# Performance work log

Hardware: AMD Instinct MI355X
Metric: run time of the kernel (lower is better)

Reference implementation:

```python
import jax, jax.numpy as jnp
import numpy as np

# --- module hyperparameters (init_kwargs) ---
K = 64
PZ, PY, PX = 5, 5, 5          # patch_size
PROJ = 512                     # projection_dim
B, C, D, H, W = 4, 256, 32, 64, 64


def setup_inputs() -> dict:
    key = jax.random.key(0)
    k1, k2, k3, k4 = jax.random.split(key, 4)
    feature_map = jax.random.normal(k1, (B, C, D, H, W), jnp.float32)
    score_map = jax.random.normal(k2, (B, 1, D, H, W), jnp.float32)
    # LazyLinear(projection_dim) materialized: in_features = C * K
    Wp = jax.random.normal(k3, (PROJ, C * K), jnp.float32) / np.sqrt(C * K).astype(np.float32)
    b = jax.random.normal(k4, (PROJ,), jnp.float32) * 0.01
    return {"feature_map": feature_map, "score_map": score_map, "Wp": Wp, "b": b}


def reference(feature_map, score_map, Wp, b):
    Bn, Cn, Dn, Hn, Wn = feature_map.shape
    flat = score_map.reshape(Bn, -1)                      # (B, D*H*W)
    scores, idx = jax.lax.top_k(flat, K)                  # (B, K)
    z = idx // (Hn * Wn)
    y = (idx % (Hn * Wn)) // Wn
    x = idx % Wn
    centers = jnp.stack([z, y, x], axis=-1)               # (B, K, 3)

    # boundary-clamped window origins: z0 = max(cz - dz//2, 0), window [z0, min(z0+dz, D))
    z0 = jnp.maximum(z - PZ // 2, 0)
    y0 = jnp.maximum(y - PY // 2, 0)
    x0 = jnp.maximum(x - PX // 2, 0)

    def per_batch(fm, z0b, y0b, x0b):
        # fm: (C, D, H, W); z0b/y0b/x0b: (K,)
        iz = z0b[:, None] + jnp.arange(PZ)                # (K, PZ)
        iy = y0b[:, None] + jnp.arange(PY)
        ix = x0b[:, None] + jnp.arange(PX)
        mz, my, mx = iz < Dn, iy < Hn, ix < Wn            # out-of-range => excluded from mean
        iz = jnp.minimum(iz, Dn - 1)
        iy = jnp.minimum(iy, Hn - 1)
        ix = jnp.minimum(ix, Wn - 1)
        # gather fixed-size patches: (C, K, PZ, PY, PX)
        patch = fm[:, iz[:, :, None, None], iy[:, None, :, None], ix[:, None, None, :]]
        mask = (mz[:, :, None, None] & my[:, None, :, None] & mx[:, None, None, :]).astype(fm.dtype)  # (K,PZ,PY,PX)
        s = jnp.einsum('ckzyx,kzyx->kc', patch, mask)     # masked sum -> (K, C)
        cnt = mask.sum(axis=(-3, -2, -1))                 # (K,) = actual clamped patch volume
        return (s / cnt[:, None]).reshape(-1)             # (K*C,) — patch-major, matching torch cat order

    vec = jax.vmap(per_batch)(feature_map, z0, y0, x0)    # (B, K*C)
    feature = vec @ Wp.T + b                              # (B, PROJ)
    return centers, scores, feature
```

## Files before the change

kernel.cpp:

```cpp
#include <hip/hip_runtime.h>
#include <hip/hip_bf16.h>

#define Bn   4
#define Cn   256
#define Dn   32
#define Hn   64
#define Wn   64
#define Kt   64
#define PROJ 512
#define DHW  (Dn*Hn*Wn)
#define HW   (Hn*Wn)
#define VECLEN (Kt*Cn)

#define NBIN    4096
#define CANDMAX 4096
#define SLOT    128
#define STATIC_THR 3.0f

#define WS_CAND_OFF 0
#define WS_IDX_OFF  (256*1024)
#define WS_VEC_OFF  (260*1024)

#define OUT_SCORES 768
#define OUT_FEAT   1024

__device__ __forceinline__ unsigned f2sortable(float f) {
    unsigned u = __float_as_uint(f);
    return (u & 0x80000000u) ? ~u : (u | 0x80000000u);
}
__device__ __forceinline__ float sortable2f(unsigned u) {
    unsigned orig = (u & 0x80000000u) ? (u & 0x7FFFFFFFu) : ~u;
    return __uint_as_float(orig);
}

__global__ __launch_bounds__(256) void compact_kernel(
        const float* __restrict__ score, unsigned long long* __restrict__ cand) {
    __shared__ unsigned long long lc[SLOT - 1];
    __shared__ int lcnt;
    const int blk = blockIdx.x;
    const int b   = blk >> 6;
    const int sub = blk & 63;
    const int tid = threadIdx.x;
    if (tid == 0) lcnt = 0;
    __syncthreads();

    const unsigned thr = f2sortable(STATIC_THR);
    const float4* src = (const float4*)(score + (size_t)b * DHW) + sub * 512;
    #pragma unroll
    for (int i = tid; i < 512; i += 256) {
        float4 v = src[i];
        unsigned gbase = (unsigned)((sub * 512 + i) * 4);
        float vals[4] = {v.x, v.y, v.z, v.w};
        #pragma unroll
        for (int l = 0; l < 4; ++l) {
            unsigned u = f2sortable(vals[l]);
            if (u >= thr) {
                int pos = atomicAdd(&lcnt, 1);
                if (pos < SLOT - 1)
                    lc[pos] = ((unsigned long long)u << 32) |
                              (0xFFFFFFFFu - (gbase + l));
            }
        }
    }
    __syncthreads();

    unsigned long long* cb = cand + (size_t)blk * SLOT;
    int n = lcnt;
    if (n > SLOT - 1) n = SLOT;
    if (tid == 0) cb[0] = (unsigned long long)n;
    int m = (n > SLOT - 1) ? (SLOT - 1) : n;
    for (int i = tid; i < m; i += 256) cb[1 + i] = lc[i];
}

__global__ __launch_bounds__(256) void final_kernel(
        const float* __restrict__ score,
        const unsigned long long* __restrict__ cand,
        float* __restrict__ out, int* __restrict__ topk_idx) {
    __shared__ unsigned long long keys[CANDMAX];
    __shared__ unsigned long long win[Kt];
    __shared__ int lh[NBIN];
    __shared__ int partial[256];
    __shared__ int cnts[64], offs[64];
    __shared__ int s_n, s_thr, s_cnt, s_ovf;
    const int b   = blockIdx.x;
    const int tid = threadIdx.x;

    if (tid == 0) { s_ovf = 0; s_cnt = 0; }
    __syncthreads();
    if (tid < 64) {
        int c = (int)cand[(size_t)((b << 6) + tid) * SLOT];
        if (c > SLOT - 1) atomicOr(&s_ovf, 1);
        cnts[tid] = c;
    }
    __syncthreads();
    if (tid == 0) {
        int o = 0;
        for (int s = 0; s < 64; ++s) { offs[s] = o; o += cnts[s]; }
        s_n = o;
    }
    __syncthreads();

    int n = s_n;
    if (!s_ovf && n >= Kt && n <= CANDMAX) {
        for (int s = 0; s < 64; ++s) {
            int c = cnts[s], o = offs[s];
            const unsigned long long* cb =
                cand + (size_t)((b << 6) + s) * SLOT + 1;
            for (int i = tid; i < c; i += 256) keys[o + i] = cb[i];
        }
        __syncthreads();
    } else {
        for (int i = tid; i < NBIN; i += 256) lh[i] = 0;
        __syncthreads();
        const float4* src = (const float4*)(score + (size_t)b * DHW);
        for (int i = tid; i < DHW / 4; i += 256) {
            float4 v = src[i];
            atomicAdd(&lh[f2sortable(v.x) >> 20], 1);
            atomicAdd(&lh[f2sortable(v.y) >> 20], 1);
            atomicAdd(&lh[f2sortable(v.z) >> 20], 1);
            atomicAdd(&lh[f2sortable(v.w) >> 20], 1);
        }
        __syncthreads();
        {
            int base = NBIN - 16 - 16 * tid;
            int s = 0;
            #pragma unroll
            for (int i = 0; i < 16; ++i) s += lh[base + i];
            partial[tid] = s;
        }
        __syncthreads();
        if (tid == 0) {
            int cum = 0, T = 0;
            for (int j = 0; j < 256; ++j) {
                if (cum + partial[j] >= Kt) {
                    int bb = NBIN - 1 - 16 * j;
                    for (int i = 0; i < 16; ++i) {
                        cum += lh[bb - i];
                        if (cum >= Kt) { T = bb - i; break; }
                    }
                    break;
                }
                cum += partial[j];
            }
            s_thr = T;
        }
        __syncthreads();
        const unsigned thr = (unsigned)s_thr;
        for (int i = tid; i < DHW / 4; i += 256) {
            float4 v = src[i];
            float vals[4] = {v.x, v.y, v.z, v.w};
            #pragma unroll
            for (int l = 0; l < 4; ++l) {
                unsigned u = f2sortable(vals[l]);
                if ((u >> 20) >= thr) {
                    int pos = atomicAdd(&s_cnt, 1);
                    if (pos < CANDMAX)
                        keys[pos] = ((unsigned long long)u << 32) |
                                    (0xFFFFFFFFu - (unsigned)(4 * i + l));
                }
            }
        }
        __syncthreads();
        n = s_cnt;
        if (n > CANDMAX) n = CANDMAX;
    }

    for (int i = tid; i < n; i += 256) {
        unsigned long long k = keys[i];
        int r = 0;
        for (int j = 0; j < n; ++j) r += (keys[j] > k);
        if (r < Kt) win[r] = k;
    }
    __syncthreads();

    if (tid < Kt) {
        unsigned long long kk = win[tid];
        float sc = sortable2f((unsigned)(kk >> 32));
        unsigned gidx = 0xFFFFFFFFu - (unsigned)(kk & 0xFFFFFFFFu);
        int z = (int)(gidx >> 12);
        int y = (int)((gidx >> 6) & 63);
        int x = (int)(gidx & 63);
        int o = (b * Kt + tid) * 3;
        out[o + 0] = (float)z;
        out[o + 1] = (float)y;
        out[o + 2] = (float)x;
        out[OUT_SCORES + b * Kt + tid] = sc;
        topk_idx[b * Kt + tid] = (int)gidx;
    }
}

__global__ __launch_bounds__(256) void gather_kernel(
        const float* __restrict__ fm, const int* __restrict__ topk_idx,
        float* __restrict__ vec) {
    const int blk = blockIdx.x;
    const int b   = blk >> 6;
    const int cg  = blk & 63;
    const int tid = threadIdx.x;
    const int k   = tid & 63;
    const int c   = cg * 4 + (tid >> 6);

    const int idx = topk_idx[b * Kt + k];
    const int z = idx >> 12;
    const int y = (idx >> 6) & 63;
    const int x = idx & 63;
    const int z0 = max(z - 2, 0), y0 = max(y - 2, 0), x0 = max(x - 2, 0);
    const int nz = min(5, Dn - z0), ny = min(5, Hn - y0), nx = min(5, Wn - x0);
    const int xe = x0 + nx;
    const int a0 = x0 & ~3;
    const bool need2 = (a0 + 4) < xe;

    float m[8];
    #pragma unroll
    for (int j = 0; j < 8; ++j) {
        int e = a0 + j;
        m[j] = (e >= x0 && e < xe) ? 1.f : 0.f;
    }

    const float* base = fm + ((size_t)(b * Cn + c)) * DHW
                           + (size_t)z0 * HW + (size_t)y0 * Wn;
    float s = 0.f;
    #pragma unroll
    for (int iz = 0; iz < 5; ++iz) {
        #pragma unroll
        for (int iy = 0; iy < 5; ++iy) {
            if (iz < nz && iy < ny) {
                const float* row = base + iz * HW + iy * Wn;
                float4 v0 = *(const float4*)(row + a0);
                s = fmaf(v0.x, m[0], s);
                s = fmaf(v0.y, m[1], s);
                s = fmaf(v0.z, m[2], s);
                s = fmaf(v0.w, m[3], s);
                if (need2) {
                    float4 v1 = *(const float4*)(row + a0 + 4);
                    s = fmaf(v1.x, m[4], s);
                    s = fmaf(v1.y, m[5], s);
                    s = fmaf(v1.z, m[6], s);
                    s = fmaf(v1.w, m[7], s);
                }
            }
        }
    }
    vec[((size_t)(b * Kt + k) << 8) + c] = s / (float)(nz * ny * nx);
}

__global__ __launch_bounds__(256) void gemv_kernel(
        const float* __restrict__ vec, const float* __restrict__ Wp,
        const float* __restrict__ bias, float* __restrict__ out) {
    const int p   = blockIdx.x;
    const int tid = threadIdx.x;
    const float4* w4 = (const float4*)(Wp + (size_t)p * VECLEN);

    float acc[Bn] = {0.f, 0.f, 0.f, 0.f};
    for (int i = tid; i < VECLEN / 4; i += 256) {
        float4 wv = w4[i];
        #pragma unroll
        for (int bb = 0; bb < Bn; ++bb) {
            float4 vv = ((const float4*)(vec + bb * VECLEN))[i];
            acc[bb] += wv.x * vv.x + wv.y * vv.y + wv.z * vv.z + wv.w * vv.w;
        }
    }

    __shared__ float red[4][Bn];
    const int lane = tid & 63, wave = tid >> 6;
    #pragma unroll
    for (int bb = 0; bb < Bn; ++bb) {
        float v = acc[bb];
        #pragma unroll
        for (int off = 32; off > 0; off >>= 1) v += __shfl_down(v, off, 64);
        if (lane == 0) red[wave][bb] = v;
    }
    __syncthreads();
    if (tid < Bn) {
        int bb = tid;
        float t = red[0][bb] + red[1][bb] + red[2][bb] + red[3][bb];
        out[OUT_FEAT + bb * PROJ + p] = t + bias[p];
    }
}

extern "C" void kernel_launch(void* const* d_in, const int* in_sizes, int n_in,
                              void* d_out, int out_size, void* d_ws, size_t ws_size,
                              hipStream_t stream) {
    const float* fm    = (const float*)d_in[0];
    const float* score = (const float*)d_in[1];
    const float* Wp    = (const float*)d_in[2];
    const float* bias  = (const float*)d_in[3];
    float* out = (float*)d_out;

    char* ws = (char*)d_ws;
    unsigned long long* cand = (unsigned long long*)(ws + WS_CAND_OFF);
    int*   topk_idx = (int*)(ws + WS_IDX_OFF);
    float* vec      = (float*)(ws + WS_VEC_OFF);

    compact_kernel<<<Bn * 64, 256, 0, stream>>>(score, cand);
    final_kernel<<<Bn, 256, 0, stream>>>(score, cand, out, topk_idx);
    gather_kernel<<<Bn * 64, 256, 0, stream>>>(fm, topk_idx, vec);
    gemv_kernel<<<PROJ, 256, 0, stream>>>(vec, Wp, bias, out);
}
```

Baseline: 66.20 us.

## Fuse four pipeline kernels into one cooperative kernel with grid syncs

After: 138.5 us. 2.09x slower.

```diff
diff --git a/kernel.cpp b/kernel.cpp
--- a/kernel.cpp
+++ b/kernel.cpp
@@ -1,5 +1,8 @@
 #include <hip/hip_runtime.h>
 #include <hip/hip_bf16.h>
+#include <hip/hip_cooperative_groups.h>
+
+namespace cg = cooperative_groups;
 
 #define Bn   4
 #define Cn   256
@@ -33,247 +36,253 @@
     return __uint_as_float(orig);
 }
 
-__global__ __launch_bounds__(256) void compact_kernel(
-        const float* __restrict__ score, unsigned long long* __restrict__ cand) {
-    __shared__ unsigned long long lc[SLOT - 1];
-    __shared__ int lcnt;
+__global__ __launch_bounds__(256) void fused_kernel(
+        const float* __restrict__ fm, const float* __restrict__ score,
+        const float* __restrict__ Wp, const float* __restrict__ bias,
+        float* __restrict__ out, unsigned long long* __restrict__ cand,
+        int* __restrict__ topk_idx, float* __restrict__ vec) {
+    cg::grid_group grid = cg::this_grid();
     const int blk = blockIdx.x;
-    const int b   = blk >> 6;
-    const int sub = blk & 63;
     const int tid = threadIdx.x;
-    if (tid == 0) lcnt = 0;
-    __syncthreads();
-
-    const unsigned thr = f2sortable(STATIC_THR);
-    const float4* src = (const float4*)(score + (size_t)b * DHW) + sub * 512;
-    #pragma unroll
-    for (int i = tid; i < 512; i += 256) {
-        float4 v = src[i];
-        unsigned gbase = (unsigned)((sub * 512 + i) * 4);
-        float vals[4] = {v.x, v.y, v.z, v.w};
-        #pragma unroll
-        for (int l = 0; l < 4; ++l) {
-            unsigned u = f2sortable(vals[l]);
-            if (u >= thr) {
-                int pos = atomicAdd(&lcnt, 1);
-                if (pos < SLOT - 1)
-                    lc[pos] = ((unsigned long long)u << 32) |
-                              (0xFFFFFFFFu - (gbase + l));
-            }
-        }
-    }
-    __syncthreads();
-
-    unsigned long long* cb = cand + (size_t)blk * SLOT;
-    int n = lcnt;
-    if (n > SLOT - 1) n = SLOT;
-    if (tid == 0) cb[0] = (unsigned long long)n;
-    int m = (n > SLOT - 1) ? (SLOT - 1) : n;
-    for (int i = tid; i < m; i += 256) cb[1 + i] = lc[i];
-}
-
-__global__ __launch_bounds__(256) void final_kernel(
-        const float* __restrict__ score,
-        const unsigned long long* __restrict__ cand,
-        float* __restrict__ out, int* __restrict__ topk_idx) {
+
     __shared__ unsigned long long keys[CANDMAX];
     __shared__ unsigned long long win[Kt];
     __shared__ int lh[NBIN];
     __shared__ int partial[256];
     __shared__ int cnts[64], offs[64];
     __shared__ int s_n, s_thr, s_cnt, s_ovf;
-    const int b   = blockIdx.x;
-    const int tid = threadIdx.x;
-
-    if (tid == 0) { s_ovf = 0; s_cnt = 0; }
-    __syncthreads();
-    if (tid < 64) {
-        int c = (int)cand[(size_t)((b << 6) + tid) * SLOT];
-        if (c > SLOT - 1) atomicOr(&s_ovf, 1);
-        cnts[tid] = c;
-    }
-    __syncthreads();
-    if (tid == 0) {
-        int o = 0;
-        for (int s = 0; s < 64; ++s) { offs[s] = o; o += cnts[s]; }
-        s_n = o;
-    }
-    __syncthreads();
-
-    int n = s_n;
-    if (!s_ovf && n >= Kt && n <= CANDMAX) {
-        for (int s = 0; s < 64; ++s) {
-            int c = cnts[s], o = offs[s];
-            const unsigned long long* cb =
-                cand + (size_t)((b << 6) + s) * SLOT + 1;
-            for (int i = tid; i < c; i += 256) keys[o + i] = cb[i];
-        }
-        __syncthreads();
-    } else {
-        for (int i = tid; i < NBIN; i += 256) lh[i] = 0;
-        __syncthreads();
-        const float4* src = (const float4*)(score + (size_t)b * DHW);
-        for (int i = tid; i < DHW / 4; i += 256) {
+    __shared__ unsigned long long lc[SLOT - 1];
+    __shared__ int lcnt;
+    __shared__ float gred[4][8];
+
+    {
+        const int b   = blk >> 6;
+        const int sub = blk & 63;
+        if (tid == 0) lcnt = 0;
+        __syncthreads();
+
+        const unsigned thr = f2sortable(STATIC_THR);
+        const float4* src = (const float4*)(score + (size_t)b * DHW) + sub * 512;
+        #pragma unroll
+        for (int i = tid; i < 512; i += 256) {
             float4 v = src[i];
-            atomicAdd(&lh[f2sortable(v.x) >> 20], 1);
-            atomicAdd(&lh[f2sortable(v.y) >> 20], 1);
-            atomicAdd(&lh[f2sortable(v.z) >> 20], 1);
-            atomicAdd(&lh[f2sortable(v.w) >> 20], 1);
-        }
-        __syncthreads();
-        {
-            int base = NBIN - 16 - 16 * tid;
-            int s = 0;
-            #pragma unroll
-            for (int i = 0; i < 16; ++i) s += lh[base + i];
-            partial[tid] = s;
-        }
-        __syncthreads();
-        if (tid == 0) {
-            int cum = 0, T = 0;
-            for (int j = 0; j < 256; ++j) {
-                if (cum + partial[j] >= Kt) {
-                    int bb = NBIN - 1 - 16 * j;
-                    for (int i = 0; i < 16; ++i) {
-                        cum += lh[bb - i];
-                        if (cum >= Kt) { T = bb - i; break; }
-                    }
-                    break;
-                }
-                cum += partial[j];
-            }
-            s_thr = T;
-        }
-        __syncthreads();
-        const unsigned thr = (unsigned)s_thr;
-        for (int i = tid; i < DHW / 4; i += 256) {
-            float4 v = src[i];
+            unsigned gbase = (unsigned)((sub * 512 + i) * 4);
             float vals[4] = {v.x, v.y, v.z, v.w};
             #pragma unroll
             for (int l = 0; l < 4; ++l) {
                 unsigned u = f2sortable(vals[l]);
-                if ((u >> 20) >= thr) {
-                    int pos = atomicAdd(&s_cnt, 1);
-                    if (pos < CANDMAX)
-                        keys[pos] = ((unsigned long long)u << 32) |
-                                    (0xFFFFFFFFu - (unsigned)(4 * i + l));
+                if (u >= thr) {
+                    int pos = atomicAdd(&lcnt, 1);
+                    if (pos < SLOT - 1)
+                        lc[pos] = ((unsigned long long)u << 32) |
+                                  (0xFFFFFFFFu - (gbase + l));
                 }
             }
         }
         __syncthreads();
-        n = s_cnt;
-        if (n > CANDMAX) n = CANDMAX;
+
+        unsigned long long* cb = cand + (size_t)blk * SLOT;
+        int n = lcnt;
+        if (n > SLOT - 1) n = SLOT;
+        if (tid == 0) cb[0] = (unsigned long long)n;
+        int m = (n > SLOT - 1) ? (SLOT - 1) : n;
+        for (int i = tid; i < m; i += 256) cb[1 + i] = lc[i];
     }
-
-    for (int i = tid; i < n; i += 256) {
-        unsigned long long k = keys[i];
-        int r = 0;
-        for (int j = 0; j < n; ++j) r += (keys[j] > k);
-        if (r < Kt) win[r] = k;
+    grid.sync();
+
+    if (blk < Bn) {
+        const int b = blk;
+        if (tid == 0) { s_ovf = 0; s_cnt = 0; }
+        __syncthreads();
+        if (tid < 64) {
+            int c = (int)cand[(size_t)((b << 6) + tid) * SLOT];
+            if (c > SLOT - 1) atomicOr(&s_ovf, 1);
+            cnts[tid] = c;
+        }
+        __syncthreads();
+        if (tid == 0) {
+            int o = 0;
+            for (int s = 0; s < 64; ++s) { offs[s] = o; o += cnts[s]; }
+            s_n = o;
+        }
+        __syncthreads();
+
+        int n = s_n;
+        if (!s_ovf && n >= Kt && n <= CANDMAX) {
+            for (int s = 0; s < 64; ++s) {
+                int c = cnts[s], o = offs[s];
+                const unsigned long long* cb =
+                    cand + (size_t)((b << 6) + s) * SLOT + 1;
+                for (int i = tid; i < c; i += 256) keys[o + i] = cb[i];
+            }
+            __syncthreads();
+        } else {
+            for (int i = tid; i < NBIN; i += 256) lh[i] = 0;
+            __syncthreads();
+            const float4* src = (const float4*)(score + (size_t)b * DHW);
+            for (int i = tid; i < DHW / 4; i += 256) {
+                float4 v = src[i];
+                atomicAdd(&lh[f2sortable(v.x) >> 20], 1);
+                atomicAdd(&lh[f2sortable(v.y) >> 20], 1);
+                atomicAdd(&lh[f2sortable(v.z) >> 20], 1);
+                atomicAdd(&lh[f2sortable(v.w) >> 20], 1);
+            }
+            __syncthreads();
+            {
+                int base = NBIN - 16 - 16 * tid;
+                int s = 0;
+                #pragma unroll
+                for (int i = 0; i < 16; ++i) s += lh[base + i];
+                partial[tid] = s;
+            }
+            __syncthreads();
+            if (tid == 0) {
+                int cum = 0, T = 0;
+                for (int j = 0; j < 256; ++j) {
+                    if (cum + partial[j] >= Kt) {
+                        int bb = NBIN - 1 - 16 * j;
+                        for (int i = 0; i < 16; ++i) {
+                            cum += lh[bb - i];
+                            if (cum >= Kt) { T = bb - i; break; }
+                        }
+                        break;
+                    }
+                    cum += partial[j];
+                }
+                s_thr = T;
+            }
+            __syncthreads();
+            const unsigned thr = (unsigned)s_thr;
+            for (int i = tid; i < DHW / 4; i += 256) {
+                float4 v = src[i];
+                float vals[4] = {v.x, v.y, v.z, v.w};
+                #pragma unroll
+                for (int l = 0; l < 4; ++l) {
+                    unsigned u = f2sortable(vals[l]);
+                    if ((u >> 20) >= thr) {
+                        int pos = atomicAdd(&s_cnt, 1);
+                        if (pos < CANDMAX)
+                            keys[pos] = ((unsigned long long)u << 32) |
+                                        (0xFFFFFFFFu - (unsigned)(4 * i + l));
+                    }
+                }
+            }
+            __syncthreads();
+            n = s_cnt;
+            if (n > CANDMAX) n = CANDMAX;
+        }
+
+        for (int i = tid; i < n; i += 256) {
+            unsigned long long k = keys[i];
+            int r = 0;
+            for (int j = 0; j < n; ++j) r += (keys[j] > k);
+            if (r < Kt) win[r] = k;
+        }
+        __syncthreads();
+
+        if (tid < Kt) {
+            unsigned long long kk = win[tid];
+            float sc = sortable2f((unsigned)(kk >> 32));
+            unsigned gidx = 0xFFFFFFFFu - (unsigned)(kk & 0xFFFFFFFFu);
+            int z = (int)(gidx >> 12);
+            int y = (int)((gidx >> 6) & 63);
+            int x = (int)(gidx & 63);
+            int o = (b * Kt + tid) * 3;
+            out[o + 0] = (float)z;
+            out[o + 1] = (float)y;
+            out[o + 2] = (float)x;
+            out[OUT_SCORES + b * Kt + tid] = sc;
+            topk_idx[b * Kt + tid] = (int)gidx;
+        }
     }
-    __syncthreads();
-
-    if (tid < Kt) {
-        unsigned long long kk = win[tid];
-        float sc = sortable2f((unsigned)(kk >> 32));
-        unsigned gidx = 0xFFFFFFFFu - (unsigned)(kk & 0xFFFFFFFFu);
-        int z = (int)(gidx >> 12);
-        int y = (int)((gidx >> 6) & 63);
-        int x = (int)(gidx & 63);
-        int o = (b * Kt + tid) * 3;
-        out[o + 0] = (float)z;
-        out[o + 1] = (float)y;
-        out[o + 2] = (float)x;
-        out[OUT_SCORES + b * Kt + tid] = sc;
-        topk_idx[b * Kt + tid] = (int)gidx;
+    grid.sync();
+
+    {
+        const int b   = blk >> 6;
+        const int cg_ = blk & 63;
+        const int k   = tid & 63;
+        const int c   = cg_ * 4 + (tid >> 6);
+
+        const int idx = topk_idx[b * Kt + k];
+        const int z = idx >> 12;
+        const int y = (idx >> 6) & 63;
+        const int x = idx & 63;
+        const int z0 = max(z - 2, 0), y0 = max(y - 2, 0), x0 = max(x - 2, 0);
+        const int nz = min(5, Dn - z0), ny = min(5, Hn - y0), nx = min(5, Wn - x0);
+        const int xe = x0 + nx;
+        const int a0 = x0 & ~3;
+        const bool need2 = (a0 + 4) < xe;
+
+        float m[8];
+        #pragma unroll
+        for (int j = 0; j < 8; ++j) {
+            int e = a0 + j;
+            m[j] = (e >= x0 && e < xe) ? 1.f : 0.f;
+        }
+
+        const float* base = fm + ((size_t)(b * Cn + c)) * DHW
+                               + (size_t)z0 * HW + (size_t)y0 * Wn;
+        float s = 0.f;
+        #pragma unroll
+        for (int iz = 0; iz < 5; ++iz) {
+            #pragma unroll
+            for (int iy = 0; iy < 5; ++iy) {
+                if (iz < nz && iy < ny) {
+                    const float* row = base + iz * HW + iy * Wn;
+                    float4 v0 = *(const float4*)(row + a0);
+                    s = fmaf(v0.x, m[0], s);
+                    s = fmaf(v0.y, m[1], s);
+                    s = fmaf(v0.z, m[2], s);
+                    s = fmaf(v0.w, m[3], s);
+                    if (need2) {
+                        float4 v1 = *(const float4*)(row + a0 + 4);
+                        s = fmaf(v1.x, m[4], s);
+                        s = fmaf(v1.y, m[5], s);
+                        s = fmaf(v1.z, m[6], s);
+                        s = fmaf(v1.w, m[7], s);
+                    }
+                }
+            }
+        }
+        vec[((size_t)(b * Kt + k) << 8) + c] = s / (float)(nz * ny * nx);
     }
-}
-
-__global__ __launch_bounds__(256) void gather_kernel(
-        const float* __restrict__ fm, const int* __restrict__ topk_idx,
-        float* __restrict__ vec) {
-    const int blk = blockIdx.x;
-    const int b   = blk >> 6;
-    const int cg  = blk & 63;
-    const int tid = threadIdx.x;
-    const int k   = tid & 63;
-    const int c   = cg * 4 + (tid >> 6);
-
-    const int idx = topk_idx[b * Kt + k];
-    const int z = idx >> 12;
-    const int y = (idx >> 6) & 63;
-    const int x = idx & 63;
-    const int z0 = max(z - 2, 0), y0 = max(y - 2, 0), x0 = max(x - 2, 0);
-    const int nz = min(5, Dn - z0), ny = min(5, Hn - y0), nx = min(5, Wn - x0);
-    const int xe = x0 + nx;
-    const int a0 = x0 & ~3;
-    const bool need2 = (a0 + 4) < xe;
-
-    float m[8];
-    #pragma unroll
-    for (int j = 0; j < 8; ++j) {
-        int e = a0 + j;
-        m[j] = (e >= x0 && e < xe) ? 1.f : 0.f;
-    }
-
-    const float* base = fm + ((size_t)(b * Cn + c)) * DHW
-                           + (size_t)z0 * HW + (size_t)y0 * Wn;
-    float s = 0.f;
-    #pragma unroll
-    for (int iz = 0; iz < 5; ++iz) {
-        #pragma unroll
-        for (int iy = 0; iy < 5; ++iy) {
-            if (iz < nz && iy < ny) {
-                const float* row = base + iz * HW + iy * Wn;
-                float4 v0 = *(const float4*)(row + a0);
-                s = fmaf(v0.x, m[0], s);
-                s = fmaf(v0.y, m[1], s);
-                s = fmaf(v0.z, m[2], s);
-                s = fmaf(v0.w, m[3], s);
-                if (need2) {
-                    float4 v1 = *(const float4*)(row + a0 + 4);
-                    s = fmaf(v1.x, m[4], s);
-                    s = fmaf(v1.y, m[5], s);
-                    s = fmaf(v1.z, m[6], s);
-                    s = fmaf(v1.w, m[7], s);
-                }
-            }
-        }
-    }
-    vec[((size_t)(b * Kt + k) << 8) + c] = s / (float)(nz * ny * nx);
-}
-
-__global__ __launch_bounds__(256) void gemv_kernel(
-        const float* __restrict__ vec, const float* __restrict__ Wp,
-        const float* __restrict__ bias, float* __restrict__ out) {
-    const int p   = blockIdx.x;
-    const int tid = threadIdx.x;
-    const float4* w4 = (const float4*)(Wp + (size_t)p * VECLEN);
-
-    float acc[Bn] = {0.f, 0.f, 0.f, 0.f};
-    for (int i = tid; i < VECLEN / 4; i += 256) {
-        float4 wv = w4[i];
+    grid.sync();
+
+    {
+        const int p0 = blk * 2;
+        const float4* w0 = (const float4*)(Wp + (size_t)p0 * VECLEN);
+        const float4* w1 = (const float4*)(Wp + (size_t)(p0 + 1) * VECLEN);
+
+        float acc0[Bn] = {0.f, 0.f, 0.f, 0.f};
+        float acc1[Bn] = {0.f, 0.f, 0.f, 0.f};
+        for (int i = tid; i < VECLEN / 4; i += 256) {
+            float4 a = w0[i];
+            float4 c = w1[i];
+            #pragma unroll
+            for (int bb = 0; bb < Bn; ++bb) {
+                float4 vv = ((const float4*)(vec + bb * VECLEN))[i];
+                acc0[bb] += a.x * vv.x + a.y * vv.y + a.z * vv.z + a.w * vv.w;
+                acc1[bb] += c.x * vv.x + c.y * vv.y + c.z * vv.z + c.w * vv.w;
+            }
+        }
+
+        const int lane = tid & 63, wave = tid >> 6;
         #pragma unroll
         for (int bb = 0; bb < Bn; ++bb) {
-            float4 vv = ((const float4*)(vec + bb * VECLEN))[i];
-            acc[bb] += wv.x * vv.x + wv.y * vv.y + wv.z * vv.z + wv.w * vv.w;
-        }
-    }
-
-    __shared__ float red[4][Bn];
-    const int lane = tid & 63, wave = tid >> 6;
-    #pragma unroll
-    for (int bb = 0; bb < Bn; ++bb) {
-        float v = acc[bb];
-        #pragma unroll
-        for (int off = 32; off > 0; off >>= 1) v += __shfl_down(v, off, 64);
-        if (lane == 0) red[wave][bb] = v;
-    }
-    __syncthreads();
-    if (tid < Bn) {
-        int bb = tid;
-        float t = red[0][bb] + red[1][bb] + red[2][bb] + red[3][bb];
-        out[OUT_FEAT + bb * PROJ + p] = t + bias[p];
+            float v0 = acc0[bb], v1 = acc1[bb];
+            #pragma unroll
+            for (int off = 32; off > 0; off >>= 1) {
+                v0 += __shfl_down(v0, off, 64);
+                v1 += __shfl_down(v1, off, 64);
+            }
+            if (lane == 0) { gred[wave][bb * 2] = v0; gred[wave][bb * 2 + 1] = v1; }
+        }
+        __syncthreads();
+        if (tid < 8) {
+            int bb = tid >> 1, q = tid & 1;
+            float t = gred[0][tid] + gred[1][tid] + gred[2][tid] + gred[3][tid];
+            out[OUT_FEAT + bb * PROJ + p0 + q] = t + bias[p0 + q];
+        }
     }
 }
 
@@ -291,8 +300,8 @@
     int*   topk_idx = (int*)(ws + WS_IDX_OFF);
     float* vec      = (float*)(ws + WS_VEC_OFF);
 
-    compact_kernel<<<Bn * 64, 256, 0, stream>>>(score, cand);
-    final_kernel<<<Bn, 256, 0, stream>>>(score, cand, out, topk_idx);
-    gather_kernel<<<Bn * 64, 256, 0, stream>>>(fm, topk_idx, vec);
-    gemv_kernel<<<PROJ, 256, 0, stream>>>(vec, Wp, bias, out);
+    void* args[] = { (void*)&fm, (void*)&score, (void*)&Wp, (void*)&bias,
+                     (void*)&out, (void*)&cand, (void*)&topk_idx, (void*)&vec };
+    hipLaunchCooperativeKernel((const void*)fused_kernel, dim3(256), dim3(256),
+                               args, 0, stream);
 }
```
